# Kernel tuning notes

Hardware: AMD Instinct MI355X
Metric: run time of the kernel (lower is better)

The kernel has to match this reference:

```python
import jax, jax.numpy as jnp
import numpy as np

N, E = 10000, 100000
WIDTH, KER_WIDTH, DEPTH = 32, 128, 3
EDGE_ATTR_DIM, IN_WIDTH, OUT_WIDTH, COORD_DIM = 6, 3, 1, 3


def _glorot(k, fan_in, fan_out):
    return jax.random.normal(k, (fan_in, fan_out), jnp.float32) / np.sqrt(fan_in).astype(np.float32)


def setup_inputs() -> dict:
    key = jax.random.key(0)
    ks = jax.random.split(key, 16)
    z = lambda n: jnp.zeros((n,), jnp.float32)
    return {
        "x": jax.random.normal(ks[0], (N, IN_WIDTH), jnp.float32),
        "edge_index": jax.random.randint(ks[1], (2, E), 0, N),
        "edge_attr": jax.random.normal(ks[2], (E, EDGE_ATTR_DIM), jnp.float32),
        "coords_init": jax.random.normal(ks[3], (N, COORD_DIM), jnp.float32),
        "fc1_w": _glorot(ks[4], IN_WIDTH, WIDTH), "fc1_b": z(WIDTH),
        "ker_w1": _glorot(ks[5], EDGE_ATTR_DIM + 1, KER_WIDTH // 2), "ker_b1": z(KER_WIDTH // 2),
        "ker_w2": _glorot(ks[6], KER_WIDTH // 2, KER_WIDTH), "ker_b2": z(KER_WIDTH),
        "ker_w3": _glorot(ks[7], KER_WIDTH, WIDTH * WIDTH), "ker_b3": z(WIDTH * WIDTH),
        "cm_w1": _glorot(ks[8], WIDTH, WIDTH), "cm_b1": z(WIDTH),
        "cm_w2": _glorot(ks[9], WIDTH, 1) * 1e-3,  # xavier gain=0.001 coord head, no bias
        "fc2_w1": _glorot(ks[10], WIDTH, 2 * WIDTH), "fc2_b1": z(2 * WIDTH),
        "fc2_w2": _glorot(ks[11], 2 * WIDTH, OUT_WIDTH), "fc2_b2": z(OUT_WIDTH),
    }


def _seg_mean(data, seg, n):
    s = jax.ops.segment_sum(data, seg, num_segments=n)
    c = jax.ops.segment_sum(jnp.ones((seg.shape[0], 1), data.dtype), seg, num_segments=n)
    return s / jnp.clip(c, 1.0)


def reference(x, edge_index, edge_attr, coords_init,
              fc1_w, fc1_b, ker_w1, ker_b1, ker_w2, ker_b2, ker_w3, ker_b3,
              cm_w1, cm_b1, cm_w2, fc2_w1, fc2_b1, fc2_w2, fc2_b2):
    row, col = edge_index[0], edge_index[1]
    h = x @ fc1_w + fc1_b                                   # [N, W]
    coord = coords_init
    for _ in range(DEPTH):
        coord_diff = coord[row] - coord[col]                # [E, 3]
        radial = jnp.sum(coord_diff * coord_diff, axis=-1, keepdims=True)
        kin = jnp.concatenate([edge_attr, radial], axis=-1)  # [E, ker_in]
        k = jax.nn.relu(kin @ ker_w1 + ker_b1)
        k = jax.nn.relu(k @ ker_w2 + ker_b2)
        Wk = (k @ ker_w3 + ker_b3).reshape(E, WIDTH, WIDTH)  # per-edge kernel matrix
        m = jnp.einsum('eij,ej->ei', Wk, h[col])             # per-edge message [E, W]
        phi = jax.nn.relu(m @ cm_w1 + cm_b1) @ cm_w2         # [E, 1]
        coord = coord + _seg_mean(coord_diff * phi, row, N)  # equivariant coord update
        h = jax.nn.relu(h + _seg_mean(m, row, N))            # GKN node update
    out = jax.nn.relu(h @ fc2_w1 + fc2_b1) @ fc2_w2 + fc2_b2  # [N, out_width]
    return out, coord
```

## Files before the change

### kernel.cpp

```cpp
#include <hip/hip_runtime.h>
#include <hip/hip_bf16.h>

#define NN 10000
#define NE 100000

typedef __bf16 bf16x8 __attribute__((ext_vector_type(8)));
typedef float  f32x4  __attribute__((ext_vector_type(4)));
typedef unsigned int u32x4 __attribute__((ext_vector_type(4)));

__device__ __forceinline__ f32x4 relu4(f32x4 a) {
    a.x = fmaxf(a.x, 0.f); a.y = fmaxf(a.y, 0.f);
    a.z = fmaxf(a.z, 0.f); a.w = fmaxf(a.w, 0.f);
    return a;
}


__global__ void k_setup(const float* __restrict__ w3, __bf16* __restrict__ w3sw,
                        const float* __restrict__ w2, __bf16* __restrict__ w2sw,
                        const float* __restrict__ x, const float* __restrict__ fc1w,
                        const float* __restrict__ fc1b, const float* __restrict__ cinit,
                        float* __restrict__ h, float* __restrict__ coord,
                        const int* __restrict__ eidx, int* __restrict__ deg) {
    int t = blockIdx.x * blockDim.x + threadIdx.x;
    if (t < 131072) {
        int jj = t & 7;
        int L  = (t >> 3) & 63;
        int ks = (t >> 9) & 3;
        int jt = (t >> 11) & 1;
        int i  = t >> 12;
        int c    = ks*32 + (L >> 4)*8 + jj;
        int colv = i*32 + jt*16 + (L & 15);
        w3sw[t] = (__bf16)w3[c*1024 + colv];
    } else if (t < 139264) {
        int u = t - 131072;
        int jj = u & 7;
        int L  = (u >> 3) & 63;
        int ks = (u >> 9) & 1;
        int nt = u >> 10;
        int c1 = ks*32 + (L >> 4)*8 + jj;
        int c2 = nt*16 + (L & 15);
        w2sw[u] = (__bf16)w2[c1*128 + c2];
    } else if (t < 139264 + NN) {
        int n = t - 139264;
        float x0 = x[n*3+0], x1 = x[n*3+1], x2 = x[n*3+2];
        #pragma unroll
        for (int j = 0; j < 32; j += 4) {
            f32x4 a = *(const f32x4*)(fc1b + j);
            a += x0 * (*(const f32x4*)(fc1w + 0*32 + j));
            a += x1 * (*(const f32x4*)(fc1w + 1*32 + j));
            a += x2 * (*(const f32x4*)(fc1w + 2*32 + j));
            *(f32x4*)(h + n*32 + j) = a;
        }
        coord[n*3+0] = cinit[n*3+0];
        coord[n*3+1] = cinit[n*3+1];
        coord[n*3+2] = cinit[n*3+2];
    } else if (t < 139264 + NN + NE) {
        int e = t - 139264 - NN;
        atomicAdd(&deg[eidx[e]], 1);
    }
}

__global__ __launch_bounds__(1024, 1)
void k_scan(const int* __restrict__ deg, int* __restrict__ rowptr,
            int* __restrict__ cursor, float* __restrict__ deg_inv) {
    __shared__ int ssum[1024];
    const int tid = threadIdx.x;
    const int CH = 10;
    const int base = tid * CH;
    int s = 0;
    for (int i = 0; i < CH; ++i) { int n = base + i; if (n < NN) s += deg[n]; }
    ssum[tid] = s;
    __syncthreads();
    for (int off = 1; off < 1024; off <<= 1) {
        int t = (tid >= off) ? ssum[tid - off] : 0;
        __syncthreads();
        ssum[tid] += t;
        __syncthreads();
    }
    int run = ssum[tid] - s;
    for (int i = 0; i < CH; ++i) {
        int n = base + i;
        if (n < NN) {
            int d = deg[n];
            rowptr[n] = run; cursor[n] = run; run += d;
            deg_inv[n] = 1.0f / (float)(d > 1 ? d : 1);
        }
    }
    if (tid == 1023) rowptr[NN] = ssum[1023];
}

__global__ void k_fill(const int* __restrict__ eidx, int* __restrict__ cursor,
                       int* __restrict__ pos_r) {
    int e = blockIdx.x * blockDim.x + threadIdx.x;
    if (e < NE) {
        int r = eidx[e];
        pos_r[e] = atomicAdd(&cursor[r], 1);
    }
}

__global__ __launch_bounds__(256, 2)
void k_layer(const float* __restrict__ coord, const int* __restrict__ eidx,
             const float* __restrict__ eattr,
             const float* __restrict__ w1, const float* __restrict__ b1,
             const __bf16* __restrict__ w2sw, const float* __restrict__ b2,
             const __bf16* __restrict__ w3sw, const float* __restrict__ b3,
             const float* __restrict__ h,
             const float* __restrict__ cm_w1, const float* __restrict__ cm_b1,
             const float* __restrict__ cm_w2, const int* __restrict__ pos_r,
             float* __restrict__ cds, float* __restrict__ m_s,
             float* __restrict__ phis) {
    __shared__ unsigned smem_u[9216];
    __bf16* kt1 = (__bf16*)smem_u;
    __bf16* kt2 = (__bf16*)smem_u + 10240;
    const int lane = threadIdx.x & 63;
    const int wave = threadIdx.x >> 6;
    const int q = lane >> 4, t = lane & 15;
    const int base = blockIdx.x * 64;

    const int eg = base + lane;
    const int egc = eg < NE ? eg : NE - 1;
    const bool wvalid = eg < NE;
    const int pos = pos_r[egc];

    int col = eidx[NE + egc];
    float hcol[32];
    {
        const f32x4* hp = (const f32x4*)(h + (size_t)col * 32);
        #pragma unroll
        for (int v = 0; v < 8; ++v) {
            f32x4 hv = hp[v];
            hcol[v*4+0] = hv.x; hcol[v*4+1] = hv.y; hcol[v*4+2] = hv.z; hcol[v*4+3] = hv.w;
        }
    }
    bf16x8 bcur[8];
    {
        const __bf16* wb0 = w3sw + (size_t)(wave * 8) * 4096;
        #pragma unroll
        for (int f = 0; f < 8; ++f)
            bcur[f] = *(const bf16x8*)(wb0 + (f*64 + lane) * 8);
    }

    {
        int r = eidx[egc];
        float dx = coord[r*3+0] - coord[col*3+0];
        float dy = coord[r*3+1] - coord[col*3+1];
        float dz = coord[r*3+2] - coord[col*3+2];
        float rad = dx*dx + dy*dy + dz*dz;
        if (wave == 0 && wvalid) {
            f32x4 cdv = {dx, dy, dz, rad};
            *(f32x4*)(cds + (size_t)pos*4) = cdv;
        }
        float kin[7];
        #pragma unroll
        for (int a = 0; a < 6; ++a) kin[a] = eattr[(size_t)egc*6 + a];
        kin[6] = rad;

        const int g0 = wave * 16;
        f32x4 acc1[4];
        #pragma unroll
        for (int g = 0; g < 4; ++g) acc1[g] = *(const f32x4*)(b1 + g0 + g*4);
        #pragma unroll
        for (int t7 = 0; t7 < 7; ++t7) {
            float kv = kin[t7];
            #pragma unroll
            for (int g = 0; g < 4; ++g)
                acc1[g] += kv * (*(const f32x4*)(w1 + t7*64 + g0 + g*4));
        }
        #pragma unroll
        for (int cc = 0; cc < 2; ++cc) {
            f32x4 a0 = relu4(acc1[cc*2]), a1 = relu4(acc1[cc*2+1]);
            bf16x8 pk = {(__bf16)a0.x, (__bf16)a0.y, (__bf16)a0.z, (__bf16)a0.w,
                         (__bf16)a1.x, (__bf16)a1.y, (__bf16)a1.z, (__bf16)a1.w};
            int chunk = wave*2 + cc;
            *(bf16x8*)(kt1 + lane*72 + ((chunk ^ (lane & 7)) * 8)) = pk;
        }
    }
    __syncthreads();

    {
        bf16x8 af[4][2];
        #pragma unroll
        for (int mt = 0; mt < 4; ++mt) {
            int ep = mt*16 + t;
            #pragma unroll
            for (int ks = 0; ks < 2; ++ks)
                af[mt][ks] = *(const bf16x8*)(kt1 + ep*72 + (((ks*4 + q) ^ (ep & 7)) * 8));
        }
        #pragma unroll
        for (int nn = 0; nn < 2; ++nn) {
            int nt = wave*2 + nn;
            f32x4 a2[4];
            #pragma unroll
            for (int mt = 0; mt < 4; ++mt) a2[mt] = (f32x4){0.f, 0.f, 0.f, 0.f};
            #pragma unroll
            for (int ks = 0; ks < 2; ++ks) {
                bf16x8 bf_ = *(const bf16x8*)(w2sw + ((nt*2 + ks)*64 + lane) * 8);
                #pragma unroll
                for (int mt = 0; mt < 4; ++mt)
                    a2[mt] = __builtin_amdgcn_mfma_f32_16x16x32_bf16(af[mt][ks], bf_, a2[mt], 0, 0, 0);
            }
            float bias = b2[nt*16 + t];
            int chunk = nt*2 + (t >> 3);
            int tin = t & 7;
            #pragma unroll
            for (int mt = 0; mt < 4; ++mt) {
                #pragma unroll
                for (int rr = 0; rr < 4; ++rr) {
                    int row = mt*16 + q*4 + rr;
                    kt2[row*128 + ((chunk ^ (row & 15)) * 8) + tin] =
                        (__bf16)fmaxf(a2[mt][rr] + bias, 0.f);
                }
            }
        }
    }
    __syncthreads();

    bf16x8 afrag[4][4];
    #pragma unroll
    for (int mt = 0; mt < 4; ++mt) {
        int ep = mt*16 + t;
        #pragma unroll
        for (int ks = 0; ks < 4; ++ks) {
            int ck = ks*4 + q;
            afrag[mt][ks] = *(const bf16x8*)(kt2 + ep*128 + ((ck ^ (ep & 15)) * 8));
        }
    }

    unsigned* wkw = smem_u + wave * 1280;
    const unsigned* wkrow = wkw + lane * 20;
    const int maskr = (lane ^ (lane >> 3)) & 3;
    float mv[8];

    #pragma unroll
    for (int ii = 0; ii < 8; ++ii) {
        const int i = wave * 8 + ii;
        f32x4 acc[4][2];
        #pragma unroll
        for (int mt = 0; mt < 4; ++mt) {
            acc[mt][0] = (f32x4){0.f, 0.f, 0.f, 0.f};
            acc[mt][1] = (f32x4){0.f, 0.f, 0.f, 0.f};
        }
        #pragma unroll
        for (int jt = 0; jt < 2; ++jt) {
            #pragma unroll
            for (int ks = 0; ks < 4; ++ks) {
                bf16x8 bfrag = bcur[jt*4 + ks];
                #pragma unroll
                for (int mt = 0; mt < 4; ++mt)
                    acc[mt][jt] = __builtin_amdgcn_mfma_f32_16x16x32_bf16(
                        afrag[mt][ks], bfrag, acc[mt][jt], 0, 0, 0);
            }
        }
        if (ii < 7) {
            const __bf16* wbn = w3sw + (size_t)(i + 1) * 4096;
            #pragma unroll
            for (int f = 0; f < 8; ++f)
                bcur[f] = *(const bf16x8*)(wbn + (f*64 + lane) * 8);
        }
        float bias0 = b3[i*32 + t];
        float bias1 = b3[i*32 + 16 + t];
        #pragma unroll
        for (int mt = 0; mt < 4; ++mt) {
            #pragma unroll
            for (int r = 0; r < 4; ++r) {
                int row = mt*16 + q*4 + r;
                float a0 = acc[mt][0][r] + bias0;
                float a1 = acc[mt][1][r] + bias1;
                unsigned u0 = (unsigned)__builtin_bit_cast(unsigned short, (__bf16)a0);
                unsigned u1 = (unsigned)__builtin_bit_cast(unsigned short, (__bf16)a1);
                int msk = (row ^ (row >> 3)) & 3;
                wkw[row*20 + ((((t >> 2) ^ msk) << 2) | (t & 3))] = u0 | (u1 << 16);
            }
        }
        float s = 0.f;
        #pragma unroll
        for (int j = 0; j < 4; ++j) {
            u32x4 wv = *(const u32x4*)(wkrow + ((j ^ maskr) << 2));
            #pragma unroll
            for (int k = 0; k < 4; ++k) {
                unsigned w = wv[k];
                int c = j*4 + k;
                float flo = __uint_as_float(w << 16);
                float fhi = __uint_as_float(w & 0xFFFF0000u);
                s += flo * hcol[c] + fhi * hcol[16 + c];
            }
        }
        mv[ii] = s;
    }

    if (wvalid) {
        f32x4 v0 = {mv[0], mv[1], mv[2], mv[3]};
        f32x4 v1 = {mv[4], mv[5], mv[6], mv[7]};
        *(f32x4*)(m_s + (size_t)pos*32 + wave*8)     = v0;
        *(f32x4*)(m_s + (size_t)pos*32 + wave*8 + 4) = v1;
    }

    __syncthreads();
    float* mvx = (float*)smem_u;
    #pragma unroll
    for (int ii = 0; ii < 8; ++ii)
        mvx[(wave*8 + ii)*65 + lane] = mv[ii];
    __syncthreads();
    if (wave == 0) {
        float m2[32];
        #pragma unroll
        for (int i = 0; i < 32; ++i) m2[i] = mvx[i*65 + lane];
        float phi = 0.f;
        for (int o = 0; o < 32; o += 4) {
            f32x4 a = *(const f32x4*)(cm_b1 + o);
            #pragma unroll
            for (int i = 0; i < 32; ++i)
                a += m2[i] * (*(const f32x4*)(cm_w1 + i*32 + o));
            a = relu4(a);
            f32x4 w2 = *(const f32x4*)(cm_w2 + o);
            phi += a.x*w2.x + a.y*w2.y + a.z*w2.z + a.w*w2.w;
        }
        if (wvalid) phis[pos] = phi;
    }
}

__global__ __launch_bounds__(256, 4)
void k_gather(const int* __restrict__ rowptr,
              const float* __restrict__ m_s, const float* __restrict__ phis,
              const float* __restrict__ cds, const float* __restrict__ deg_inv,
              float* __restrict__ coord, float* __restrict__ h,
              const float* __restrict__ fw1, const float* __restrict__ fb1,
              const float* __restrict__ fw2, const float* __restrict__ fb2,
              float* __restrict__ out, int dofinal) {
    int tid = blockIdx.x * blockDim.x + threadIdx.x;
    int n = tid >> 3, sub = tid & 7;
    if (n >= NN) return;
    int st = rowptr[n], en = rowptr[n+1];
    f32x4 am0 = {0.f, 0.f, 0.f, 0.f}, am1 = {0.f, 0.f, 0.f, 0.f};
    int p = st;
    for (; p + 1 < en; p += 2) {
        am0 += *(const f32x4*)(m_s + (size_t)p*32 + sub*4);
        am1 += *(const f32x4*)(m_s + (size_t)(p+1)*32 + sub*4);
    }
    if (p < en) am0 += *(const f32x4*)(m_s + (size_t)p*32 + sub*4);
    f32x4 am = am0 + am1;

    float di = deg_inv[n];
    f32x4 hv = *(const f32x4*)(h + (size_t)n*32 + sub*4);
    hv = relu4(hv + am * di);

    float c0 = 0.f, c1 = 0.f, c2 = 0.f;
    if (sub == 0) {
        float cx0 = 0.f, cy0 = 0.f, cz0 = 0.f;
        float cx1 = 0.f, cy1 = 0.f, cz1 = 0.f;
        int pp = st;
        for (; pp + 1 < en; pp += 2) {
            f32x4 cd0 = *(const f32x4*)(cds + (size_t)pp*4);
            f32x4 cd1 = *(const f32x4*)(cds + (size_t)(pp+1)*4);
            float p0 = phis[pp], p1 = phis[pp+1];
            cx0 += cd0.x * p0; cy0 += cd0.y * p0; cz0 += cd0.z * p0;
            cx1 += cd1.x * p1; cy1 += cd1.y * p1; cz1 += cd1.z * p1;
        }
        if (pp < en) {
            f32x4 cd0 = *(const f32x4*)(cds + (size_t)pp*4);
            float p0 = phis[pp];
            cx0 += cd0.x * p0; cy0 += cd0.y * p0; cz0 += cd0.z * p0;
        }
        c0 = coord[n*3+0] + (cx0 + cx1) * di;
        c1 = coord[n*3+1] + (cy0 + cy1) * di;
        c2 = coord[n*3+2] + (cz0 + cz1) * di;
    }

    if (!dofinal) {
        *(f32x4*)(h + (size_t)n*32 + sub*4) = hv;
        if (sub == 0) {
            coord[n*3+0] = c0; coord[n*3+1] = c1; coord[n*3+2] = c2;
        }
        return;
    }

    const int gbase = (tid & 63) & 56;
    float hreg[32];
    #pragma unroll
    for (int s2 = 0; s2 < 8; ++s2) {
        hreg[s2*4+0] = __shfl(hv.x, gbase + s2, 64);
        hreg[s2*4+1] = __shfl(hv.y, gbase + s2, 64);
        hreg[s2*4+2] = __shfl(hv.z, gbase + s2, 64);
        hreg[s2*4+3] = __shfl(hv.w, gbase + s2, 64);
    }
    float po = 0.f;
    #pragma unroll
    for (int oo = 0; oo < 8; oo += 4) {
        int o = sub*8 + oo;
        f32x4 a = *(const f32x4*)(fb1 + o);
        #pragma unroll
        for (int i = 0; i < 32; ++i)
            a += hreg[i] * (*(const f32x4*)(fw1 + i*64 + o));
        a = relu4(a);
        f32x4 w2 = *(const f32x4*)(fw2 + o);
        po += a.x*w2.x + a.y*w2.y + a.z*w2.z + a.w*w2.w;
    }
    po += __shfl_xor(po, 1, 64);
    po += __shfl_xor(po, 2, 64);
    po += __shfl_xor(po, 4, 64);
    if (sub == 0) {
        out[n] = po + fb2[0];
        out[NN + n*3 + 0] = c0;
        out[NN + n*3 + 1] = c1;
        out[NN + n*3 + 2] = c2;
    }
}


extern "C" void kernel_launch(void* const* d_in, const int* in_sizes, int n_in,
                              void* d_out, int out_size, void* d_ws, size_t ws_size,
                              hipStream_t stream) {
    const float* x      = (const float*)d_in[0];
    const int*   eidx   = (const int*)  d_in[1];
    const float* eattr  = (const float*)d_in[2];
    const float* cinit  = (const float*)d_in[3];
    const float* fc1w   = (const float*)d_in[4];
    const float* fc1b   = (const float*)d_in[5];
    const float* kw1    = (const float*)d_in[6];
    const float* kb1    = (const float*)d_in[7];
    const float* kw2    = (const float*)d_in[8];
    const float* kb2    = (const float*)d_in[9];
    const float* kw3    = (const float*)d_in[10];
    const float* kb3    = (const float*)d_in[11];
    const float* cmw1   = (const float*)d_in[12];
    const float* cmb1   = (const float*)d_in[13];
    const float* cmw2   = (const float*)d_in[14];
    const float* f2w1   = (const float*)d_in[15];
    const float* f2b1   = (const float*)d_in[16];
    const float* f2w2   = (const float*)d_in[17];
    const float* f2b2   = (const float*)d_in[18];
    float* out = (float*)d_out;

    char* p = (char*)d_ws;
    auto carve = [&](size_t bytes) {
        void* r = (void*)p;
        p += (bytes + 255) & ~(size_t)255;
        return r;
    };
    float*  h        = (float*) carve((size_t)NN * 32 * 4);
    float*  coord    = (float*) carve((size_t)NN * 3 * 4);
    int*    deg      = (int*)   carve((size_t)NN * 4);
    float*  deg_inv  = (float*) carve((size_t)NN * 4);
    int*    rowptr   = (int*)   carve((size_t)(NN + 1) * 4);
    int*    cursor   = (int*)   carve((size_t)NN * 4);
    int*    pos_r    = (int*)   carve((size_t)NE * 4);
    float*  cds      = (float*) carve((size_t)NE * 4 * 4);
    float*  m_s      = (float*) carve((size_t)NE * 32 * 4);
    float*  phis     = (float*) carve((size_t)NE * 4);
    __bf16* w3sw     = (__bf16*)carve((size_t)131072 * 2);
    __bf16* w2sw     = (__bf16*)carve((size_t)8192 * 2);

    const int TB = 256;
    dim3 gE((NE + TB - 1) / TB), b(TB);
    dim3 gS((139264 + NN + NE + TB - 1) / TB);
    dim3 gG((NE + 63) / 64);
    dim3 gA((NN*8 + TB - 1) / TB);

    hipMemsetAsync(deg, 0, (size_t)NN * 4, stream);
    k_setup<<<gS, b, 0, stream>>>(kw3, w3sw, kw2, w2sw, x, fc1w, fc1b, cinit,
                                  h, coord, eidx, deg);
    k_scan <<<1, dim3(1024), 0, stream>>>(deg, rowptr, cursor, deg_inv);
    k_fill <<<gE, b, 0, stream>>>(eidx, cursor, pos_r);

    for (int d = 0; d < 3; ++d) {
        k_layer<<<gG, b, 0, stream>>>(coord, eidx, eattr, kw1, kb1, w2sw, kb2,
                                      w3sw, kb3, h, cmw1, cmb1, cmw2, pos_r,
                                      cds, m_s, phis);
        k_gather<<<gA, b, 0, stream>>>(rowptr, m_s, phis, cds, deg_inv, coord, h,
                                       f2w1, f2b1, f2w2, f2b2, out, d == 2 ? 1 : 0);
    }
}
```

Before: 342.5 us.

## Fold CSR fill into degree count and overlap shared memory buffers

The degree-counting atomic in setup now records each edge's slot within its row, so the separate fill kernel and cursor array are gone and each layer computes the position as rowptr plus that slot. The layer kernel's shared buffer shrinks from 36 KB to 26 KB by letting the second hidden tile overlap storage later reused for per-wave kernel weights. An extra barrier after the fragment loads guards that reuse. This removes one launch and may allow more resident blocks per CU, at the cost of an extra rowptr gather per edge and an extra sync per block.

After: 332.2 us. -3.0%, faster.

```diff
diff --git a/kernel.cpp b/kernel.cpp
--- a/kernel.cpp
+++ b/kernel.cpp
@@ -20,7 +20,8 @@
                         const float* __restrict__ x, const float* __restrict__ fc1w,
                         const float* __restrict__ fc1b, const float* __restrict__ cinit,
                         float* __restrict__ h, float* __restrict__ coord,
-                        const int* __restrict__ eidx, int* __restrict__ deg) {
+                        const int* __restrict__ eidx, int* __restrict__ deg,
+                        int* __restrict__ within) {
     int t = blockIdx.x * blockDim.x + threadIdx.x;
     if (t < 131072) {
         int jj = t & 7;
@@ -56,13 +57,13 @@
         coord[n*3+2] = cinit[n*3+2];
     } else if (t < 139264 + NN + NE) {
         int e = t - 139264 - NN;
-        atomicAdd(&deg[eidx[e]], 1);
+        within[e] = atomicAdd(&deg[eidx[e]], 1);
     }
 }
 
 __global__ __launch_bounds__(1024, 1)
 void k_scan(const int* __restrict__ deg, int* __restrict__ rowptr,
-            int* __restrict__ cursor, float* __restrict__ deg_inv) {
+            float* __restrict__ deg_inv) {
     __shared__ int ssum[1024];
     const int tid = threadIdx.x;
     const int CH = 10;
@@ -82,20 +83,11 @@
         int n = base + i;
         if (n < NN) {
             int d = deg[n];
-            rowptr[n] = run; cursor[n] = run; run += d;
+            rowptr[n] = run; run += d;
             deg_inv[n] = 1.0f / (float)(d > 1 ? d : 1);
         }
     }
     if (tid == 1023) rowptr[NN] = ssum[1023];
-}
-
-__global__ void k_fill(const int* __restrict__ eidx, int* __restrict__ cursor,
-                       int* __restrict__ pos_r) {
-    int e = blockIdx.x * blockDim.x + threadIdx.x;
-    if (e < NE) {
-        int r = eidx[e];
-        pos_r[e] = atomicAdd(&cursor[r], 1);
-    }
 }
 
 __global__ __launch_bounds__(256, 2)
@@ -106,12 +98,13 @@
              const __bf16* __restrict__ w3sw, const float* __restrict__ b3,
              const float* __restrict__ h,
              const float* __restrict__ cm_w1, const float* __restrict__ cm_b1,
-             const float* __restrict__ cm_w2, const int* __restrict__ pos_r,
+             const float* __restrict__ cm_w2,
+             const int* __restrict__ rowptr, const int* __restrict__ within,
              float* __restrict__ cds, float* __restrict__ m_s,
              float* __restrict__ phis) {
-    __shared__ unsigned smem_u[9216];
+    __shared__ unsigned smem_u[6656];
     __bf16* kt1 = (__bf16*)smem_u;
-    __bf16* kt2 = (__bf16*)smem_u + 10240;
+    __bf16* kt2 = (__bf16*)smem_u + 5120;
     const int lane = threadIdx.x & 63;
     const int wave = threadIdx.x >> 6;
     const int q = lane >> 4, t = lane & 15;
@@ -120,7 +113,8 @@
     const int eg = base + lane;
     const int egc = eg < NE ? eg : NE - 1;
     const bool wvalid = eg < NE;
-    const int pos = pos_r[egc];
+    const int r_node = eidx[egc];
+    const int pos = rowptr[r_node] + within[egc];
 
     int col = eidx[NE + egc];
     float hcol[32];
@@ -141,10 +135,9 @@
     }
 
     {
-        int r = eidx[egc];
-        float dx = coord[r*3+0] - coord[col*3+0];
-        float dy = coord[r*3+1] - coord[col*3+1];
-        float dz = coord[r*3+2] - coord[col*3+2];
+        float dx = coord[r_node*3+0] - coord[col*3+0];
+        float dy = coord[r_node*3+1] - coord[col*3+1];
+        float dz = coord[r_node*3+2] - coord[col*3+2];
         float rad = dx*dx + dy*dy + dz*dz;
         if (wave == 0 && wvalid) {
             f32x4 cdv = {dx, dy, dz, rad};
@@ -225,6 +218,7 @@
             afrag[mt][ks] = *(const bf16x8*)(kt2 + ep*128 + ((ck ^ (ep & 15)) * 8));
         }
     }
+    __syncthreads();
 
     unsigned* wkw = smem_u + wave * 1280;
     const unsigned* wkrow = wkw + lane * 20;
@@ -442,8 +436,7 @@
     int*    deg      = (int*)   carve((size_t)NN * 4);
     float*  deg_inv  = (float*) carve((size_t)NN * 4);
     int*    rowptr   = (int*)   carve((size_t)(NN + 1) * 4);
-    int*    cursor   = (int*)   carve((size_t)NN * 4);
-    int*    pos_r    = (int*)   carve((size_t)NE * 4);
+    int*    within   = (int*)   carve((size_t)NE * 4);
     float*  cds      = (float*) carve((size_t)NE * 4 * 4);
     float*  m_s      = (float*) carve((size_t)NE * 32 * 4);
     float*  phis     = (float*) carve((size_t)NE * 4);
@@ -451,21 +444,20 @@
     __bf16* w2sw     = (__bf16*)carve((size_t)8192 * 2);
 
     const int TB = 256;
-    dim3 gE((NE + TB - 1) / TB), b(TB);
+    dim3 b(TB);
     dim3 gS((139264 + NN + NE + TB - 1) / TB);
     dim3 gG((NE + 63) / 64);
     dim3 gA((NN*8 + TB - 1) / TB);
 
     hipMemsetAsync(deg, 0, (size_t)NN * 4, stream);
     k_setup<<<gS, b, 0, stream>>>(kw3, w3sw, kw2, w2sw, x, fc1w, fc1b, cinit,
-                                  h, coord, eidx, deg);
-    k_scan <<<1, dim3(1024), 0, stream>>>(deg, rowptr, cursor, deg_inv);
-    k_fill <<<gE, b, 0, stream>>>(eidx, cursor, pos_r);
+                                  h, coord, eidx, deg, within);
+    k_scan <<<1, dim3(1024), 0, stream>>>(deg, rowptr, deg_inv);
 
     for (int d = 0; d < 3; ++d) {
         k_layer<<<gG, b, 0, stream>>>(coord, eidx, eattr, kw1, kb1, w2sw, kb2,
-                                      w3sw, kb3, h, cmw1, cmb1, cmw2, pos_r,
-                                      cds, m_s, phis);
+                                      w3sw, kb3, h, cmw1, cmb1, cmw2,
+                                      rowptr, within, cds, m_s, phis);
         k_gather<<<gA, b, 0, stream>>>(rowptr, m_s, phis, cds, deg_inv, coord, h,
                                        f2w1, f2b1, f2w2, f2b2, out, d == 2 ? 1 : 0);
     }
```
